# Optimization experiments

Measured on AMD Instinct MI355X. Metric: run time of the kernel, lower is better.

The kernel has to match this reference:

```python
import jax, jax.numpy as jnp
import numpy as np

B, S, F = 4, 2048, 256
H, D = 8, 32            # n_heads, width_embedding; H*D == F
LN_EPS = 1e-3           # tf.keras LayerNormalization default epsilon


def setup_inputs() -> dict:
    key = jax.random.key(0)
    ks = jax.random.split(key, 6)
    s = 1.0 / np.sqrt(F)
    return {
        "x": jax.random.normal(ks[0], (B, S, F), dtype=jnp.float32),
        "Wq": jax.random.normal(ks[1], (F, H * D), dtype=jnp.float32) * s,
        "Wk": jax.random.normal(ks[2], (F, H * D), dtype=jnp.float32) * s,
        "Wv": jax.random.normal(ks[3], (F, H * D), dtype=jnp.float32) * s,
        "Wf": jax.random.normal(ks[4], (H * D, F), dtype=jnp.float32) * s,
        "bf": jnp.zeros((F,), dtype=jnp.float32),
    }


def reference(x, Wq, Wk, Wv, Wf, bf):
    # QKV projections (no bias), split heads: [B,S,H*D] -> [B,H,S,D]
    def split(t):
        return t.reshape(B, S, H, D).transpose(0, 2, 1, 3)

    q = split(x @ Wq) / jnp.sqrt(jnp.asarray(H, x.dtype))  # NOTE: module scales by sqrt(n_heads)
    k = split(x @ Wk)
    v = split(x @ Wv)

    scores = jnp.einsum("bhsd,bhtd->bhst", q, k)          # [B,H,S,S]
    attn = jax.nn.softmax(scores, axis=-1)
    ctx = jnp.einsum("bhst,bhtd->bhsd", attn, v)           # [B,H,S,D]

    y = ctx.transpose(0, 2, 1, 3).reshape(B, S, H * D)     # merge heads
    y = jax.nn.relu(y @ Wf + bf)                            # final dense with relu

    # residual + LayerNorm(center=False, scale=False)
    z = x + y
    mean = jnp.mean(z, axis=-1, keepdims=True)
    var = jnp.var(z, axis=-1, keepdims=True)
    return (z - mean) * jax.lax.rsqrt(var + LN_EPS)
```

## Files before the change

### kernel.cpp

```cpp
#include <hip/hip_runtime.h>
#include <math.h>

#define NB 4
#define NS 2048
#define NF 256
#define NH 8
#define ND 32

constexpr float LN_EPS = 1e-3f;
constexpr float QSCALE = 0.35355339059327373f;
constexpr float LOG2E  = 1.4426950408889634f;
constexpr int   NSPLIT = 2;
constexpr int   KRANGE = NS / NSPLIT;
constexpr size_t PO_PER = (size_t)NB * NH * NS * ND;

typedef __bf16 bf16x8 __attribute__((ext_vector_type(8)));
typedef float f32x4 __attribute__((ext_vector_type(4)));

__global__ __launch_bounds__(256)
void prep_w(const float* __restrict__ Wq, const float* __restrict__ Wk,
            const float* __restrict__ Wv, const float* __restrict__ Wf,
            unsigned short* __restrict__ wt)
{
    __shared__ float tile[64][65];
    const int wid = blockIdx.x;
    const int t = threadIdx.x;
    const int z = wid >> 4;
    const int tl = wid & 15;
    const float* W = (z == 0) ? Wq : (z == 1) ? Wk : (z == 2) ? Wv : Wf;
    const float scale = (z == 0) ? QSCALE * LOG2E : 1.0f;
    const int r0 = (tl >> 2) * 64, c0 = (tl & 3) * 64;
    const int tr = t >> 4, tc4 = (t & 15) * 4;

    #pragma unroll
    for (int p = 0; p < 4; ++p) {
        float4 v = *(const float4*)(W + (size_t)(r0 + tr + p * 16) * NF + c0 + tc4);
        tile[tr + p * 16][tc4 + 0] = v.x;
        tile[tr + p * 16][tc4 + 1] = v.y;
        tile[tr + p * 16][tc4 + 2] = v.z;
        tile[tr + p * 16][tc4 + 3] = v.w;
    }
    __syncthreads();
    #pragma unroll
    for (int p = 0; p < 4; ++p) {
        union { ushort4 u; __bf16 h[4]; } o;
        #pragma unroll
        for (int j = 0; j < 4; ++j)
            o.h[j] = (__bf16)(tile[tc4 + j][tr + p * 16] * scale);
        *(ushort4*)(wt + (size_t)z * 65536 + (size_t)(c0 + tr + p * 16) * NF + r0 + tc4) = o.u;
    }
}

__global__ __launch_bounds__(256)
void qkv_mfma(const float* __restrict__ x, const unsigned short* __restrict__ wt,
              unsigned short* __restrict__ qo, unsigned short* __restrict__ ko,
              unsigned short* __restrict__ vo)
{
    const int z = blockIdx.y;
    unsigned short* out = (z == 0) ? qo : (z == 1) ? ko : vo;
    const unsigned short* W = wt + (size_t)z * 65536;

    const int r0 = blockIdx.x * 64;
    const int t = threadIdx.x;
    const int w = t >> 6, lane = t & 63;
    const int l15 = lane & 15, lhi = lane >> 4;
    const int wr = w >> 1, wc = w & 1;

    f32x4 acc[2][8] = {};

    #pragma unroll 2
    for (int kt = 0; kt < NF; kt += 32) {
        const float* xr0 = x + (size_t)(r0 + wr * 32 + l15) * NF + kt + lhi * 8;
        const float* xr1 = x + (size_t)(r0 + wr * 32 + 16 + l15) * NF + kt + lhi * 8;
        float4 f00 = *(const float4*)xr0;
        float4 f01 = *(const float4*)(xr0 + 4);
        float4 f10 = *(const float4*)xr1;
        float4 f11 = *(const float4*)(xr1 + 4);
        bf16x8 a0, a1;
        a0[0] = (__bf16)f00.x; a0[1] = (__bf16)f00.y; a0[2] = (__bf16)f00.z; a0[3] = (__bf16)f00.w;
        a0[4] = (__bf16)f01.x; a0[5] = (__bf16)f01.y; a0[6] = (__bf16)f01.z; a0[7] = (__bf16)f01.w;
        a1[0] = (__bf16)f10.x; a1[1] = (__bf16)f10.y; a1[2] = (__bf16)f10.z; a1[3] = (__bf16)f10.w;
        a1[4] = (__bf16)f11.x; a1[5] = (__bf16)f11.y; a1[6] = (__bf16)f11.z; a1[7] = (__bf16)f11.w;
        #pragma unroll
        for (int c = 0; c < 8; ++c) {
            bf16x8 b = *(const bf16x8*)(W + (size_t)(wc * 128 + c * 16 + l15) * NF + kt + lhi * 8);
            acc[0][c] = __builtin_amdgcn_mfma_f32_16x16x32_bf16(a0, b, acc[0][c], 0, 0, 0);
            acc[1][c] = __builtin_amdgcn_mfma_f32_16x16x32_bf16(a1, b, acc[1][c], 0, 0, 0);
        }
    }

    #pragma unroll
    for (int i = 0; i < 2; ++i) {
        #pragma unroll
        for (int c = 0; c < 8; ++c) {
            const int col = wc * 128 + c * 16 + l15;
            const int h = col >> 5, d = col & 31;
            const int rowbase = r0 + wr * 32 + i * 16 + lhi * 4;
            const int b = rowbase >> 11, s = rowbase & 2047;
            if (z == 2) {
                union { ushort4 u; __bf16 h4[4]; } o;
                #pragma unroll
                for (int r = 0; r < 4; ++r) o.h4[r] = (__bf16)acc[i][c][r];
                *(ushort4*)(out + ((size_t)(b * NH + h) * ND + d) * NS + s) = o.u;
            } else {
                #pragma unroll
                for (int r = 0; r < 4; ++r) {
                    __bf16 o = (__bf16)acc[i][c][r];
                    out[((size_t)(b * NH + h) * NS + (s + r)) * ND + d] = *(unsigned short*)&o;
                }
            }
        }
    }
}

__global__ __launch_bounds__(256)
void attn_mfma(const unsigned short* __restrict__ q, const unsigned short* __restrict__ k,
               const unsigned short* __restrict__ v, float* __restrict__ po,
               float* __restrict__ pl)
{
    const int bh = blockIdx.x;
    const int s0 = blockIdx.y * 128;
    const int sp = blockIdx.z;
    const int kbase = sp * KRANGE;
    const int t = threadIdx.x;
    const int w = t >> 6;
    const int lane = t & 63;
    const int l15 = lane & 15;
    const int lhi = lane >> 4;
    const int sx  = l15 & 8;
    const int vd  = w * 8 + (lane >> 3);
    const int vk  = (lane & 7) * 8;
    const int vsx = vd & 8;

    __shared__ unsigned short ps[4][32][72];
    __shared__ unsigned short vt[2][32][72];

    const unsigned short* qb  = q + (size_t)bh * NS * ND;
    const unsigned short* kb  = k + (size_t)bh * NS * ND;
    const unsigned short* vtg = v + (size_t)bh * ND * NS + (size_t)vd * NS;

    bf16x8 qf0 = *(const bf16x8*)(qb + (size_t)(s0 + w * 32 + l15) * ND + lhi * 8);
    bf16x8 qf1 = *(const bf16x8*)(qb + (size_t)(s0 + w * 32 + 16 + l15) * ND + lhi * 8);

    float lp0 = 0.f, lp1 = 0.f;
    f32x4 acc00 = {0.f,0.f,0.f,0.f}, acc01 = {0.f,0.f,0.f,0.f};
    f32x4 acc10 = {0.f,0.f,0.f,0.f}, acc11 = {0.f,0.f,0.f,0.f};

    bf16x8 kf[4];
    #pragma unroll
    for (int f = 0; f < 4; ++f)
        kf[f] = *(const bf16x8*)(kb + (size_t)(kbase + f * 16 + l15) * ND + lhi * 8);
    {
        bf16x8 vv = *(const bf16x8*)(vtg + kbase + vk);
        *(bf16x8*)&vt[0][vd][vk ^ vsx] = vv;
    }
    __syncthreads();

    int cur = 0;
    #pragma unroll 2
    for (int tI = 0; tI < 16; ++tI) {
        const int ktn = kbase + ((tI + 1) & 15) * 64;
        bf16x8 vvn = *(const bf16x8*)(vtg + ktn + vk);
        bf16x8 kn[4];
        #pragma unroll
        for (int f = 0; f < 4; ++f)
            kn[f] = *(const bf16x8*)(kb + (size_t)(ktn + f * 16 + l15) * ND + lhi * 8);

        const f32x4 zero = {0.f, 0.f, 0.f, 0.f};
        f32x4 sc0[4], sc1[4];
        __builtin_amdgcn_s_setprio(1);
        #pragma unroll
        for (int f = 0; f < 4; ++f) {
            sc0[f] = __builtin_amdgcn_mfma_f32_16x16x32_bf16(kf[f], qf0, zero, 0, 0, 0);
            sc1[f] = __builtin_amdgcn_mfma_f32_16x16x32_bf16(kf[f], qf1, zero, 0, 0, 0);
        }
        __builtin_amdgcn_s_setprio(0);

        float a0 = 0.f, a1 = 0.f;
        #pragma unroll
        for (int f = 0; f < 4; ++f) {
            float p0 = __builtin_amdgcn_exp2f(sc0[f][0]);
            float p1 = __builtin_amdgcn_exp2f(sc0[f][1]);
            float p2 = __builtin_amdgcn_exp2f(sc0[f][2]);
            float p3 = __builtin_amdgcn_exp2f(sc0[f][3]);
            union { ushort4 u; __bf16 h[4]; } pk;
            pk.h[0] = (__bf16)p0; pk.h[1] = (__bf16)p1;
            pk.h[2] = (__bf16)p2; pk.h[3] = (__bf16)p3;
            *(ushort4*)&ps[w][l15][(f * 16 + lhi * 4) ^ sx] = pk.u;
            a0 += (p0 + p1) + (p2 + p3);
        }
        #pragma unroll
        for (int f = 0; f < 4; ++f) {
            float p0 = __builtin_amdgcn_exp2f(sc1[f][0]);
            float p1 = __builtin_amdgcn_exp2f(sc1[f][1]);
            float p2 = __builtin_amdgcn_exp2f(sc1[f][2]);
            float p3 = __builtin_amdgcn_exp2f(sc1[f][3]);
            union { ushort4 u; __bf16 h[4]; } pk;
            pk.h[0] = (__bf16)p0; pk.h[1] = (__bf16)p1;
            pk.h[2] = (__bf16)p2; pk.h[3] = (__bf16)p3;
            *(ushort4*)&ps[w][16 + l15][(f * 16 + lhi * 4) ^ sx] = pk.u;
            a1 += (p0 + p1) + (p2 + p3);
        }
        lp0 += a0; lp1 += a1;

        __builtin_amdgcn_s_setprio(1);
        #pragma unroll
        for (int c = 0; c < 2; ++c) {
            const int co = (c * 32 + lhi * 8) ^ sx;
            bf16x8 pa0 = *(const bf16x8*)&ps[w][l15][co];
            bf16x8 pa1 = *(const bf16x8*)&ps[w][16 + l15][co];
            bf16x8 vf0 = *(const bf16x8*)&vt[cur][l15][co];
            bf16x8 vf1 = *(const bf16x8*)&vt[cur][16 + l15][co];
            acc00 = __builtin_amdgcn_mfma_f32_16x16x32_bf16(pa0, vf0, acc00, 0, 0, 0);
            acc01 = __builtin_amdgcn_mfma_f32_16x16x32_bf16(pa0, vf1, acc01, 0, 0, 0);
            acc10 = __builtin_amdgcn_mfma_f32_16x16x32_bf16(pa1, vf0, acc10, 0, 0, 0);
            acc11 = __builtin_amdgcn_mfma_f32_16x16x32_bf16(pa1, vf1, acc11, 0, 0, 0);
        }
        __builtin_amdgcn_s_setprio(0);

        *(bf16x8*)&vt[cur ^ 1][vd][vk ^ vsx] = vvn;
        #pragma unroll
        for (int f = 0; f < 4; ++f) kf[f] = kn[f];
        __syncthreads();
        cur ^= 1;
    }

    lp0 += __shfl_xor(lp0, 16);
    lp0 += __shfl_xor(lp0, 32);
    lp1 += __shfl_xor(lp1, 16);
    lp1 += __shfl_xor(lp1, 32);

    float* pob = po + (size_t)sp * PO_PER;
    float* plb = pl + (size_t)sp * (NB * NH * NS);
    #pragma unroll
    for (int r = 0; r < 4; ++r) {
        float li0 = __shfl(lp0, lhi * 4 + r);
        float li1 = __shfl(lp1, lhi * 4 + r);
        int row0 = s0 + w * 32 + lhi * 4 + r;
        int row1 = row0 + 16;
        float* op0 = pob + ((size_t)bh * NS + row0) * ND;
        float* op1 = pob + ((size_t)bh * NS + row1) * ND;
        op0[l15]      = acc00[r];
        op0[16 + l15] = acc01[r];
        op1[l15]      = acc10[r];
        op1[16 + l15] = acc11[r];
        if (l15 == 0) {
            plb[bh * NS + row0] = li0;
            plb[bh * NS + row1] = li1;
        }
    }
}

__global__ __launch_bounds__(256)
void combine(const float* __restrict__ po, const float* __restrict__ pl,
             unsigned short* __restrict__ ctxb)
{
    const int idx = blockIdx.x * 256 + threadIdx.x;
    const int row = idx >> 2;
    const int dd = (idx & 3) * 8;
    const float* p0 = po + (size_t)row * ND + dd;
    const float* p1 = p0 + PO_PER;
    float inv = 1.0f / (pl[row] + pl[row + NB * NH * NS]);
    float4 a0 = *(const float4*)p0;
    float4 a1 = *(const float4*)(p0 + 4);
    float4 b0 = *(const float4*)p1;
    float4 b1 = *(const float4*)(p1 + 4);
    union { ushort4 u[2]; __bf16 h[8]; } o;
    o.h[0] = (__bf16)((a0.x + b0.x) * inv);
    o.h[1] = (__bf16)((a0.y + b0.y) * inv);
    o.h[2] = (__bf16)((a0.z + b0.z) * inv);
    o.h[3] = (__bf16)((a0.w + b0.w) * inv);
    o.h[4] = (__bf16)((a1.x + b1.x) * inv);
    o.h[5] = (__bf16)((a1.y + b1.y) * inv);
    o.h[6] = (__bf16)((a1.z + b1.z) * inv);
    o.h[7] = (__bf16)((a1.w + b1.w) * inv);
    const int bh = row >> 11, s = row & 2047;
    const int b = bh >> 3, h = bh & 7;
    unsigned short* op = ctxb + ((size_t)b * NS + s) * NF + h * ND + dd;
    *(ushort4*)op = o.u[0];
    *(ushort4*)(op + 4) = o.u[1];
}

__global__ __launch_bounds__(256)
void dense_ln(const unsigned short* __restrict__ ctxb, const unsigned short* __restrict__ wft,
              const float* __restrict__ bfp, const float* __restrict__ x,
              float* __restrict__ out)
{
    const int r0 = blockIdx.x * 32;
    const int t = threadIdx.x;
    const int w = t >> 6;
    const int lane = t & 63;
    const int l15 = lane & 15;
    const int lhi = lane >> 4;

    __shared__ float zs[32][258];

    f32x4 acc[2][4] = {};

    #pragma unroll 2
    for (int kt = 0; kt < NF; kt += 32) {
        bf16x8 a0 = *(const bf16x8*)(ctxb + (size_t)(r0 + l15) * NF + kt + lhi * 8);
        bf16x8 a1 = *(const bf16x8*)(ctxb + (size_t)(r0 + 16 + l15) * NF + kt + lhi * 8);
        #pragma unroll
        for (int c = 0; c < 4; ++c) {
            bf16x8 b = *(const bf16x8*)(wft + (size_t)(w * 64 + c * 16 + l15) * NF + kt + lhi * 8);
            acc[0][c] = __builtin_amdgcn_mfma_f32_16x16x32_bf16(a0, b, acc[0][c], 0, 0, 0);
            acc[1][c] = __builtin_amdgcn_mfma_f32_16x16x32_bf16(a1, b, acc[1][c], 0, 0, 0);
        }
    }

    #pragma unroll
    for (int i = 0; i < 2; ++i) {
        #pragma unroll
        for (int c = 0; c < 4; ++c) {
            const int col = w * 64 + c * 16 + l15;
            const float bb = bfp[col];
            #pragma unroll
            for (int r = 0; r < 4; ++r) {
                const int row = i * 16 + lhi * 4 + r;
                zs[row][col] = fmaxf(acc[i][c][r] + bb, 0.0f);
            }
        }
    }
    __syncthreads();

    #pragma unroll
    for (int i = 0; i < 8; ++i) {
        const int row = w * 8 + i;
        float4 yv = *(const float4*)&zs[row][lane * 4];
        float4 xv = *(const float4*)(x + (size_t)(r0 + row) * NF + lane * 4);
        float z0 = xv.x + yv.x, z1 = xv.y + yv.y;
        float z2 = xv.z + yv.z, z3 = xv.w + yv.w;
        float sum = z0 + z1 + z2 + z3;
        float sq  = z0*z0 + z1*z1 + z2*z2 + z3*z3;
        #pragma unroll
        for (int o = 1; o < 64; o <<= 1) {
            sum += __shfl_xor(sum, o);
            sq  += __shfl_xor(sq, o);
        }
        float mean = sum * (1.0f / NF);
        float var  = sq * (1.0f / NF) - mean * mean;
        float rstd = rsqrtf(var + LN_EPS);
        float4 o4;
        o4.x = (z0 - mean) * rstd;
        o4.y = (z1 - mean) * rstd;
        o4.z = (z2 - mean) * rstd;
        o4.w = (z3 - mean) * rstd;
        *(float4*)(out + (size_t)(r0 + row) * NF + lane * 4) = o4;
    }
}

extern "C" void kernel_launch(void* const* d_in, const int* in_sizes, int n_in,
                              void* d_out, int out_size, void* d_ws, size_t ws_size,
                              hipStream_t stream)
{
    const float* x  = (const float*)d_in[0];
    const float* Wq = (const float*)d_in[1];
    const float* Wk = (const float*)d_in[2];
    const float* Wv = (const float*)d_in[3];
    const float* Wf = (const float*)d_in[4];
    const float* bf = (const float*)d_in[5];
    float* out = (float*)d_out;

    const size_t per = (size_t)NB * NH * NS * ND;
    unsigned short* q    = (unsigned short*)d_ws;
    unsigned short* kk   = q + per;
    unsigned short* vv   = kk + per;
    unsigned short* wt   = vv + per;
    unsigned short* ctxb = wt + 4 * 65536;
    float* po = (float*)(ctxb + per);
    float* pl = po + (size_t)NSPLIT * PO_PER;

    prep_w<<<dim3(64), 256, 0, stream>>>(Wq, Wk, Wv, Wf, wt);
    qkv_mfma<<<dim3(128, 3), 256, 0, stream>>>(x, wt, q, kk, vv);
    attn_mfma<<<dim3(NB * NH, NS / 128, NSPLIT), 256, 0, stream>>>(q, kk, vv, po, pl);
    combine<<<dim3((NB * NS * NF / 8) / 256), 256, 0, stream>>>(po, pl, ctxb);
    dense_ln<<<dim3((NB * NS) / 32), 256, 0, stream>>>(ctxb, wt + 3 * 65536, bf, x, out);
}
```

Baseline: 84.73 us.

## Keep attention probabilities in registers by permuting K row loading

Reorders which key rows each lane loads so that the exp'd score MFMA outputs already match the A-operand layout of the PV MFMA. The per-wave shared-memory staging buffer for P is removed, along with its LDS writes and reads. V fragment reads are hoisted ahead of the MFMA block. The cost is a permuted key-row mapping, which must stay consistent with how V columns are indexed.

```diff
diff --git a/kernel.cpp b/kernel.cpp
--- a/kernel.cpp
+++ b/kernel.cpp
@@ -132,13 +132,15 @@
     const int vk  = (lane & 7) * 8;
     const int vsx = vd & 8;
 
-    __shared__ unsigned short ps[4][32][72];
     __shared__ unsigned short vt[2][32][72];
 
     const unsigned short* qb  = q + (size_t)bh * NS * ND;
     const unsigned short* kb  = k + (size_t)bh * NS * ND;
     const unsigned short* vtg = v + (size_t)bh * ND * NS + (size_t)vd * NS;
 
+    const int krow = (l15 >> 2) * 8 + (l15 & 3);
+    const unsigned short* kbp = kb + (size_t)krow * ND + lhi * 8;
+
     bf16x8 qf0 = *(const bf16x8*)(qb + (size_t)(s0 + w * 32 + l15) * ND + lhi * 8);
     bf16x8 qf1 = *(const bf16x8*)(qb + (size_t)(s0 + w * 32 + 16 + l15) * ND + lhi * 8);
 
@@ -147,9 +149,10 @@
     f32x4 acc10 = {0.f,0.f,0.f,0.f}, acc11 = {0.f,0.f,0.f,0.f};
 
     bf16x8 kf[4];
-    #pragma unroll
-    for (int f = 0; f < 4; ++f)
-        kf[f] = *(const bf16x8*)(kb + (size_t)(kbase + f * 16 + l15) * ND + lhi * 8);
+    kf[0] = *(const bf16x8*)(kbp + (size_t)kbase * ND);
+    kf[1] = *(const bf16x8*)(kbp + (size_t)kbase * ND + 128);
+    kf[2] = *(const bf16x8*)(kbp + (size_t)kbase * ND + 1024);
+    kf[3] = *(const bf16x8*)(kbp + (size_t)kbase * ND + 1152);
     {
         bf16x8 vv = *(const bf16x8*)(vtg + kbase + vk);
         *(bf16x8*)&vt[0][vd][vk ^ vsx] = vv;
@@ -162,9 +165,10 @@
         const int ktn = kbase + ((tI + 1) & 15) * 64;
         bf16x8 vvn = *(const bf16x8*)(vtg + ktn + vk);
         bf16x8 kn[4];
-        #pragma unroll
-        for (int f = 0; f < 4; ++f)
-            kn[f] = *(const bf16x8*)(kb + (size_t)(ktn + f * 16 + l15) * ND + lhi * 8);
+        kn[0] = *(const bf16x8*)(kbp + (size_t)ktn * ND);
+        kn[1] = *(const bf16x8*)(kbp + (size_t)ktn * ND + 128);
+        kn[2] = *(const bf16x8*)(kbp + (size_t)ktn * ND + 1024);
+        kn[3] = *(const bf16x8*)(kbp + (size_t)ktn * ND + 1152);
 
         const f32x4 zero = {0.f, 0.f, 0.f, 0.f};
         f32x4 sc0[4], sc1[4];
@@ -176,46 +180,46 @@
         }
         __builtin_amdgcn_s_setprio(0);
 
+        bf16x8 pa00, pa01, pa10, pa11;
         float a0 = 0.f, a1 = 0.f;
         #pragma unroll
-        for (int f = 0; f < 4; ++f) {
-            float p0 = __builtin_amdgcn_exp2f(sc0[f][0]);
-            float p1 = __builtin_amdgcn_exp2f(sc0[f][1]);
-            float p2 = __builtin_amdgcn_exp2f(sc0[f][2]);
-            float p3 = __builtin_amdgcn_exp2f(sc0[f][3]);
-            union { ushort4 u; __bf16 h[4]; } pk;
-            pk.h[0] = (__bf16)p0; pk.h[1] = (__bf16)p1;
-            pk.h[2] = (__bf16)p2; pk.h[3] = (__bf16)p3;
-            *(ushort4*)&ps[w][l15][(f * 16 + lhi * 4) ^ sx] = pk.u;
+        for (int r = 0; r < 4; ++r) {
+            float p0 = __builtin_amdgcn_exp2f(sc0[0][r]);
+            float p1 = __builtin_amdgcn_exp2f(sc0[1][r]);
+            float p2 = __builtin_amdgcn_exp2f(sc0[2][r]);
+            float p3 = __builtin_amdgcn_exp2f(sc0[3][r]);
+            pa00[r]     = (__bf16)p0;
+            pa00[4 + r] = (__bf16)p1;
+            pa01[r]     = (__bf16)p2;
+            pa01[4 + r] = (__bf16)p3;
             a0 += (p0 + p1) + (p2 + p3);
-        }
-        #pragma unroll
-        for (int f = 0; f < 4; ++f) {
-            float p0 = __builtin_amdgcn_exp2f(sc1[f][0]);
-            float p1 = __builtin_amdgcn_exp2f(sc1[f][1]);
-            float p2 = __builtin_amdgcn_exp2f(sc1[f][2]);
-            float p3 = __builtin_amdgcn_exp2f(sc1[f][3]);
-            union { ushort4 u; __bf16 h[4]; } pk;
-            pk.h[0] = (__bf16)p0; pk.h[1] = (__bf16)p1;
-            pk.h[2] = (__bf16)p2; pk.h[3] = (__bf16)p3;
-            *(ushort4*)&ps[w][16 + l15][(f * 16 + lhi * 4) ^ sx] = pk.u;
-            a1 += (p0 + p1) + (p2 + p3);
+            float s0_ = __builtin_amdgcn_exp2f(sc1[0][r]);
+            float s1_ = __builtin_amdgcn_exp2f(sc1[1][r]);
+            float s2_ = __builtin_amdgcn_exp2f(sc1[2][r]);
+            float s3_ = __builtin_amdgcn_exp2f(sc1[3][r]);
+            pa10[r]     = (__bf16)s0_;
+            pa10[4 + r] = (__bf16)s1_;
+            pa11[r]     = (__bf16)s2_;
+            pa11[4 + r] = (__bf16)s3_;
+            a1 += (s0_ + s1_) + (s2_ + s3_);
         }
         lp0 += a0; lp1 += a1;
 
+        const int co0 = (lhi * 8) ^ sx;
+        const int co1 = (32 + lhi * 8) ^ sx;
+        bf16x8 vfa0 = *(const bf16x8*)&vt[cur][l15][co0];
+        bf16x8 vfb0 = *(const bf16x8*)&vt[cur][16 + l15][co0];
+        bf16x8 vfa1 = *(const bf16x8*)&vt[cur][l15][co1];
+        bf16x8 vfb1 = *(const bf16x8*)&vt[cur][16 + l15][co1];
         __builtin_amdgcn_s_setprio(1);
-        #pragma unroll
-        for (int c = 0; c < 2; ++c) {
-            const int co = (c * 32 + lhi * 8) ^ sx;
-            bf16x8 pa0 = *(const bf16x8*)&ps[w][l15][co];
-            bf16x8 pa1 = *(const bf16x8*)&ps[w][16 + l15][co];
-            bf16x8 vf0 = *(const bf16x8*)&vt[cur][l15][co];
-            bf16x8 vf1 = *(const bf16x8*)&vt[cur][16 + l15][co];
-            acc00 = __builtin_amdgcn_mfma_f32_16x16x32_bf16(pa0, vf0, acc00, 0, 0, 0);
-            acc01 = __builtin_amdgcn_mfma_f32_16x16x32_bf16(pa0, vf1, acc01, 0, 0, 0);
-            acc10 = __builtin_amdgcn_mfma_f32_16x16x32_bf16(pa1, vf0, acc10, 0, 0, 0);
-            acc11 = __builtin_amdgcn_mfma_f32_16x16x32_bf16(pa1, vf1, acc11, 0, 0, 0);
-        }
+        acc00 = __builtin_amdgcn_mfma_f32_16x16x32_bf16(pa00, vfa0, acc00, 0, 0, 0);
+        acc01 = __builtin_amdgcn_mfma_f32_16x16x32_bf16(pa00, vfb0, acc01, 0, 0, 0);
+        acc10 = __builtin_amdgcn_mfma_f32_16x16x32_bf16(pa10, vfa0, acc10, 0, 0, 0);
+        acc11 = __builtin_amdgcn_mfma_f32_16x16x32_bf16(pa10, vfb0, acc11, 0, 0, 0);
+        acc00 = __builtin_amdgcn_mfma_f32_16x16x32_bf16(pa01, vfa1, acc00, 0, 0, 0);
+        acc01 = __builtin_amdgcn_mfma_f32_16x16x32_bf16(pa01, vfb1, acc01, 0, 0, 0);
+        acc10 = __builtin_amdgcn_mfma_f32_16x16x32_bf16(pa11, vfa1, acc10, 0, 0, 0);
+        acc11 = __builtin_amdgcn_mfma_f32_16x16x32_bf16(pa11, vfb1, acc11, 0, 0, 0);
         __builtin_amdgcn_s_setprio(0);
 
         *(bf16x8*)&vt[cur ^ 1][vd][vk ^ vsx] = vvn;
```

Measured after the change: 81.89 us. 3.4% less time.
